# Kernel tuning notes

Measured on AMD Instinct MI355X. Metric: run time of the kernel, lower is better.

Reference implementation:

```python
import jax, jax.numpy as jnp
import numpy as np

B, CH, H, W = 128, 3, 224, 224
R = 14
S = R * R  # 196 superpixels
DIMS = [11, 96, 192, 384, 768, 768]
BN_EPS = 1e-5


def setup_inputs() -> dict:
    key = jax.random.key(0)
    ks = jax.random.split(key, 64)
    inp = {}
    inp["x"] = jax.random.normal(ks[0], (B, CH, H, W), jnp.float32)
    inp["sliced"] = jax.random.randint(ks[1], (B, H, W), 0, S, jnp.int32)
    ki = 2
    for i in range(5):
        ci, co = DIMS[i], DIMS[i + 1]
        inp[f"w{i}"] = jax.random.normal(ks[ki], (co, ci), jnp.float32) / np.sqrt(ci); ki += 1
        inp[f"b{i}"] = jnp.zeros((co,), jnp.float32)
        inp[f"g{i}"] = jnp.ones((co,), jnp.float32)
        inp[f"be{i}"] = jnp.zeros((co,), jnp.float32)
        inp[f"rm{i}"] = jax.random.normal(ks[ki], (co,), jnp.float32) * 0.1; ki += 1
        inp[f"rv{i}"] = jax.random.uniform(ks[ki], (co,), jnp.float32) + 0.5; ki += 1
    return inp


def _seg_features(x, sliced):
    # x: [B,3,H,W] float, sliced: [B,H,W] int labels in [0,S)
    b, c, h, w = x.shape
    n = h * w
    ids = sliced.reshape(b, n).astype(jnp.int32)
    gid = (jnp.arange(b, dtype=jnp.int32)[:, None] * S + ids).reshape(-1)  # [B*N]

    counts = jax.ops.segment_sum(jnp.ones((b * n,), x.dtype), gid, num_segments=b * S)  # [B*S]
    rows = jnp.repeat(jnp.arange(h, dtype=x.dtype), w)
    cols = jnp.tile(jnp.arange(w, dtype=x.dtype), h)
    coords = jnp.stack([rows, cols], -1)                       # [N,2]
    coords_b = jnp.broadcast_to(coords, (b, n, 2)).reshape(b * n, 2)
    coord_sum = jax.ops.segment_sum(coords_b, gid, num_segments=b * S)  # [B*S,2]

    rgb = x.reshape(b, c, n).transpose(0, 2, 1).reshape(b * n, c)       # [B*N,3]
    rgb_sum = jax.ops.segment_sum(rgb, gid, num_segments=b * S)
    rgb_sq = jax.ops.segment_sum(rgb * rgb, gid, num_segments=b * S)

    cnt = counts[:, None]
    safe = jnp.maximum(cnt, 1.0)
    mean_coord = coord_sum / safe                              # [B*S,2]
    mean_rgb = rgb_sum / safe                                  # [B*S,3]
    # torch .std is unbiased; NaN (count<=1) replaced by 0
    var = (rgb_sq - cnt * mean_rgb * mean_rgb) / jnp.maximum(cnt - 1.0, 1.0)
    std = jnp.where(cnt > 1.0, jnp.sqrt(jnp.maximum(var, 0.0)), 0.0)

    mc = mean_coord.reshape(b, S, 2)
    mr = mean_rgb.reshape(b, S, 3)
    sd = std.reshape(b, S, 3)
    # gather pixel at the (truncated) mean location of each segment
    ri = jnp.clip(mc[..., 0].astype(jnp.int32), 0, h - 1)      # [B,S]
    ci = jnp.clip(mc[..., 1].astype(jnp.int32), 0, w - 1)
    gathered = x[jnp.arange(b)[:, None], :, ri, ci]            # [B,S,3]

    feat = jnp.concatenate([mc, mr, sd, gathered], -1)         # [B,S,11]
    feat = feat * (counts.reshape(b, S, 1) > 0).astype(x.dtype)  # absent segments stay 0
    return feat.transpose(0, 2, 1).reshape(b, 11, R, R)


def _conv_bn(h, w, b, g, be, rm, rv, act):
    # 1x1 conv == channel contraction
    h = jnp.einsum('bchw,oc->bohw', h, w) + b[None, :, None, None]
    scale = g / jnp.sqrt(rv + BN_EPS)
    h = (h - rm[None, :, None, None]) * scale[None, :, None, None] + be[None, :, None, None]
    return jax.nn.relu(h) if act else h


def reference(x, sliced,
              w0, b0, g0, be0, rm0, rv0,
              w1, b1, g1, be1, rm1, rv1,
              w2, b2, g2, be2, rm2, rv2,
              w3, b3, g3, be3, rm3, rv3,
              w4, b4, g4, be4, rm4, rv4):
    params = [(w0, b0, g0, be0, rm0, rv0), (w1, b1, g1, be1, rm1, rv1),
              (w2, b2, g2, be2, rm2, rv2), (w3, b3, g3, be3, rm3, rv3),
              (w4, b4, g4, be4, rm4, rv4)]
    h = _seg_features(x, sliced)                # [B,11,14,14]
    for i, (w, b, g, be, rm, rv) in enumerate(params):
        h = _conv_bn(h, w, b, g, be, rm, rv, act=(i < 4))  # last block: BN only
    return (sliced, h)
```

## Files before the change

kernel.cpp:

```cpp
#include <hip/hip_runtime.h>
#include <hip/hip_bf16.h>

#define HW    50176
#define IMGW  224
#define SEG   196
#define NBATCH 128
#define NCOL  (NBATCH * SEG)
#define PB    14
#define CHUNK (HW / PB)
#define VCHUNK (CHUNK / 4)

typedef __attribute__((ext_vector_type(8))) short bf16x8;
typedef __attribute__((ext_vector_type(4))) float f32x4;
typedef unsigned long long u64;

static __device__ __forceinline__ ushort f2bf(float v) {
    __hip_bfloat16 h = __float2bfloat16(v);
    return *reinterpret_cast<ushort*>(&h);
}

__global__ __launch_bounds__(256) void seg_accum(const float* __restrict__ x,
                                                 const int*   __restrict__ sl,
                                                 float*       __restrict__ stats) {
    __shared__ u64 ls[4][SEG];
    int b    = blockIdx.x / PB;
    int part = blockIdx.x % PB;
    int tid  = threadIdx.x;

    for (int i = tid; i < 4 * SEG; i += 256) (&ls[0][0])[i] = 0ull;
    __syncthreads();

    const float* xb = x + (size_t)b * 3 * HW;
    const int*   sb = sl + (size_t)b * HW;
    int v0 = part * VCHUNK;

    for (int vi = tid; vi < VCHUNK; vi += 256) {
        int vg = v0 + vi;
        int4   id4 = ((const int4*)sb)[vg];
        float4 r4  = ((const float4*)xb)[vg];
        float4 g4  = ((const float4*)(xb + HW))[vg];
        float4 b4  = ((const float4*)(xb + 2 * HW))[vg];
        int p   = vg * 4;
        int row = p / IMGW;
        int col = p - row * IMGW;
        u64 rowbits = ((u64)1 << 48) | ((u64)(unsigned)row << 24);

#pragma unroll
        for (int q = 0; q < 4; ++q) {
            int   id = (q == 0) ? id4.x : (q == 1) ? id4.y : (q == 2) ? id4.z : id4.w;
            float r  = (q == 0) ? r4.x  : (q == 1) ? r4.y  : (q == 2) ? r4.z  : r4.w;
            float g  = (q == 0) ? g4.x  : (q == 1) ? g4.y  : (q == 2) ? g4.z  : g4.w;
            float bl = (q == 0) ? b4.x  : (q == 1) ? b4.y  : (q == 2) ? b4.z  : b4.w;

            unsigned qr  = (unsigned)fmaf(r,  8192.f, 131072.5f);
            unsigned qg  = (unsigned)fmaf(g,  8192.f, 131072.5f);
            unsigned qb  = (unsigned)fmaf(bl, 8192.f, 131072.5f);
            unsigned qr2 = (unsigned)fmaf(r * r,  2048.f, 0.5f);
            unsigned qg2 = (unsigned)fmaf(g * g,  2048.f, 0.5f);
            unsigned qb2 = (unsigned)fmaf(bl * bl, 2048.f, 0.5f);

            atomicAdd(&ls[0][id], rowbits | (unsigned)(col + q));
            atomicAdd(&ls[1][id], ((u64)qg  << 32) | qr);
            atomicAdd(&ls[2][id], ((u64)qr2 << 32) | qb);
            atomicAdd(&ls[3][id], ((u64)qb2 << 32) | qg2);
        }
    }
    __syncthreads();

    const float inv_s = 1.f / 8192.f, inv_q = 1.f / 2048.f;
    for (int i = tid; i < SEG; i += 256) {
        u64 v0p = ls[0][i];
        unsigned cnt = (unsigned)(v0p >> 48);
        if (!cnt) continue;
        float fc   = (float)cnt;
        float rows = (float)((unsigned)(v0p >> 24) & 0xFFFFFFu);
        float cols = (float)((unsigned)v0p & 0xFFFFFFu);
        u64 v1 = ls[1][i], v2 = ls[2][i], v3 = ls[3][i];
        float bias = 16.f * fc;
        float rsum = (float)(unsigned)v1         * inv_s - bias;
        float gsum = (float)(unsigned)(v1 >> 32) * inv_s - bias;
        float bsum = (float)(unsigned)v2         * inv_s - bias;
        float rsq  = (float)(unsigned)(v2 >> 32) * inv_q;
        float gsq  = (float)(unsigned)v3         * inv_q;
        float bsq  = (float)(unsigned)(v3 >> 32) * inv_q;

        size_t base = (size_t)b * SEG + i;
        atomicAdd(&stats[0 * NCOL + base], fc);
        atomicAdd(&stats[1 * NCOL + base], rows);
        atomicAdd(&stats[2 * NCOL + base], cols);
        atomicAdd(&stats[3 * NCOL + base], rsum);
        atomicAdd(&stats[4 * NCOL + base], gsum);
        atomicAdd(&stats[5 * NCOL + base], bsum);
        atomicAdd(&stats[6 * NCOL + base], rsq);
        atomicAdd(&stats[7 * NCOL + base], gsq);
        atomicAdd(&stats[8 * NCOL + base], bsq);
    }
}

__global__ __launch_bounds__(256) void feat_build(const float* __restrict__ x,
                                                  const float* __restrict__ stats,
                                                  ushort*      __restrict__ F) {
    int n = blockIdx.x * 256 + threadIdx.x;
    if (n >= NCOL) return;
    int b = n / SEG;

    float cnt  = stats[n];
    float safe = fmaxf(cnt, 1.f);
    float inv  = 1.f / safe;
    float mrow = stats[1 * NCOL + n] * inv;
    float mcol = stats[2 * NCOL + n] * inv;
    float mr   = stats[3 * NCOL + n] * inv;
    float mg   = stats[4 * NCOL + n] * inv;
    float mb   = stats[5 * NCOL + n] * inv;
    float den  = fmaxf(cnt - 1.f, 1.f);
    float vr = (stats[6 * NCOL + n] - cnt * mr * mr) / den;
    float vg = (stats[7 * NCOL + n] - cnt * mg * mg) / den;
    float vb = (stats[8 * NCOL + n] - cnt * mb * mb) / den;
    bool  has2 = cnt > 1.f;
    float sr = has2 ? sqrtf(fmaxf(vr, 0.f)) : 0.f;
    float sg = has2 ? sqrtf(fmaxf(vg, 0.f)) : 0.f;
    float sb = has2 ? sqrtf(fmaxf(vb, 0.f)) : 0.f;

    int ri = min(max((int)mrow, 0), IMGW - 1);
    int ci = min(max((int)mcol, 0), IMGW - 1);
    const float* xb = x + (size_t)b * 3 * HW;
    int pi = ri * IMGW + ci;
    float gr = xb[pi], gg = xb[HW + pi], gb = xb[2 * HW + pi];

    float mask = cnt > 0.f ? 1.f : 0.f;
    ushort* Fr = F + (size_t)n * 64;
#pragma unroll
    for (int k = 11; k < 64; ++k) Fr[k] = 0;
    Fr[0]  = f2bf(mrow * mask);
    Fr[1]  = f2bf(mcol * mask);
    Fr[2]  = f2bf(mr * mask);
    Fr[3]  = f2bf(mg * mask);
    Fr[4]  = f2bf(mb * mask);
    Fr[5]  = f2bf(sr * mask);
    Fr[6]  = f2bf(sg * mask);
    Fr[7]  = f2bf(sb * mask);
    Fr[8]  = f2bf(gr * mask);
    Fr[9]  = f2bf(gg * mask);
    Fr[10] = f2bf(gb * mask);
}

__global__ __launch_bounds__(256) void convert_w(const float* __restrict__ src,
                                                 ushort* __restrict__ dst,
                                                 int Cout, int K, int Kpad, int total) {
    int i = blockIdx.x * 256 + threadIdx.x;
    if (i >= total) return;
    int o = i / Kpad, k = i - o * Kpad;
    float v = (o < Cout && k < K) ? src[(size_t)o * K + k] : 0.f;
    dst[i] = f2bf(v);
}

__global__ __launch_bounds__(256) void gemm_mfma(const ushort* __restrict__ Aact,
                                                 const ushort* __restrict__ Wb,
                                                 void* __restrict__ outp,
                                                 const float* __restrict__ bias,
                                                 const float* __restrict__ gam,
                                                 const float* __restrict__ bet,
                                                 const float* __restrict__ rm,
                                                 const float* __restrict__ rv,
                                                 int Kpad, int Cout, int OutStride,
                                                 int act, int final_out) {
    __shared__ ushort As[128 * 64];
    __shared__ ushort Bs[128 * 64];

    int tid  = threadIdx.x;
    int lane = tid & 63;
    int wid  = tid >> 6;
    int wm   = wid & 1;
    int wn   = wid >> 1;
    int n0   = blockIdx.x * 128;
    int o0   = blockIdx.y * 128;
    int mrow = lane & 15;
    int quad = lane >> 4;
    int swz  = mrow & 7;

    f32x4 acc[4][4];
#pragma unroll
    for (int i = 0; i < 4; ++i)
#pragma unroll
        for (int j = 0; j < 4; ++j) acc[i][j] = (f32x4){0.f, 0.f, 0.f, 0.f};

    int ktiles = Kpad >> 6;
    for (int kt = 0; kt < ktiles; ++kt) {
        int kb = kt * 64;
#pragma unroll
        for (int p = 0; p < 4; ++p) {
            int flat = p * 256 + tid;
            int row = flat >> 3, kg = flat & 7;
            int kgs = kg ^ (row & 7);
            const ushort* gp = Aact + (size_t)(n0 + row) * Kpad + kb + kgs * 8;
            __builtin_amdgcn_global_load_lds(
                (const __attribute__((address_space(1))) void*)gp,
                (__attribute__((address_space(3))) void*)(As + (size_t)(p * 256 + wid * 64) * 8),
                16, 0, 0);
        }
#pragma unroll
        for (int p = 0; p < 4; ++p) {
            int flat = p * 256 + tid;
            int row = flat >> 3, kg = flat & 7;
            int kgs = kg ^ (row & 7);
            const ushort* gp = Wb + (size_t)(o0 + row) * Kpad + kb + kgs * 8;
            __builtin_amdgcn_global_load_lds(
                (const __attribute__((address_space(1))) void*)gp,
                (__attribute__((address_space(3))) void*)(Bs + (size_t)(p * 256 + wid * 64) * 8),
                16, 0, 0);
        }
        __syncthreads();

#pragma unroll
        for (int ks = 0; ks < 2; ++ks) {
            bf16x8 af[4], bfr[4];
            int gbase = ks * 4 + quad;
            int slot  = (gbase ^ swz) * 8;
#pragma unroll
            for (int i = 0; i < 4; ++i)
                af[i] = *(const bf16x8*)&As[(size_t)(wm * 64 + i * 16 + mrow) * 64 + slot];
#pragma unroll
            for (int j = 0; j < 4; ++j)
                bfr[j] = *(const bf16x8*)&Bs[(size_t)(wn * 64 + j * 16 + mrow) * 64 + slot];
#pragma unroll
            for (int i = 0; i < 4; ++i)
#pragma unroll
                for (int j = 0; j < 4; ++j)
                    acc[i][j] = __builtin_amdgcn_mfma_f32_16x16x32_bf16(af[i], bfr[j], acc[i][j], 0, 0, 0);
        }
        __syncthreads();
    }

#pragma unroll
    for (int j = 0; j < 4; ++j) {
        int o = o0 + wn * 64 + j * 16 + mrow;
        float al = 0.f, bt = 0.f;
        if (o < Cout) {
            float sc = gam[o] / sqrtf(rv[o] + 1e-5f);
            al = sc;
            bt = (bias[o] - rm[o]) * sc + bet[o];
        }
#pragma unroll
        for (int i = 0; i < 4; ++i) {
            int nbase = n0 + wm * 64 + i * 16 + quad * 4;
#pragma unroll
            for (int r = 0; r < 4; ++r) {
                float v = acc[i][j][r] * al + bt;
                if (act) v = fmaxf(v, 0.f);
                int n = nbase + r;
                if (final_out) {
                    int b = n / SEG, s = n - b * SEG;
                    ((float*)outp)[(size_t)b * 768 * SEG + (size_t)o * SEG + s] = v;
                } else {
                    ((ushort*)outp)[(size_t)n * OutStride + o] = f2bf(v);
                }
            }
        }
    }
}

__global__ __launch_bounds__(256) void copy_sliced(const int4* __restrict__ sl,
                                                   float4* __restrict__ out) {
    int i = blockIdx.x * 256 + threadIdx.x;
    int4 v = sl[i];
    out[i] = make_float4((float)v.x, (float)v.y, (float)v.z, (float)v.w);
}

extern "C" void kernel_launch(void* const* d_in, const int* in_sizes, int n_in,
                              void* d_out, int out_size, void* d_ws, size_t ws_size,
                              hipStream_t stream) {
    const float* x  = (const float*)d_in[0];
    const int*   sl = (const int*)d_in[1];
    const float* Wp[5], *Bp[5], *Gp[5], *BEp[5], *RMp[5], *RVp[5];
    for (int i = 0; i < 5; ++i) {
        Wp[i]  = (const float*)d_in[2 + 6 * i + 0];
        Bp[i]  = (const float*)d_in[2 + 6 * i + 1];
        Gp[i]  = (const float*)d_in[2 + 6 * i + 2];
        BEp[i] = (const float*)d_in[2 + 6 * i + 3];
        RMp[i] = (const float*)d_in[2 + 6 * i + 4];
        RVp[i] = (const float*)d_in[2 + 6 * i + 5];
    }
    float* out = (float*)d_out;

    const int Kpad[5]  = {64, 128, 256, 384, 768};
    const int Kreal[5] = {11, 96, 192, 384, 768};
    const int Cout[5]  = {96, 192, 384, 768, 768};
    const int Opad[5]  = {128, 256, 384, 768, 768};

    char* wsb = (char*)d_ws;
    float*  stats = (float*)wsb;
    wsb += (size_t)9 * NCOL * sizeof(float);
    ushort* F = (ushort*)wsb;
    wsb += (size_t)NCOL * 64 * sizeof(ushort);
    ushort* Wpad[5];
    for (int i = 0; i < 5; ++i) {
        Wpad[i] = (ushort*)wsb;
        wsb += (size_t)Opad[i] * Kpad[i] * sizeof(ushort);
    }
    ushort* bufA = (ushort*)wsb;
    wsb += (size_t)NCOL * 384 * sizeof(ushort);
    ushort* bufB = (ushort*)wsb;

    hipMemsetAsync(stats, 0, (size_t)9 * NCOL * sizeof(float), stream);

    for (int i = 0; i < 5; ++i) {
        int total = Opad[i] * Kpad[i];
        convert_w<<<(total + 255) / 256, 256, 0, stream>>>(
            Wp[i], Wpad[i], Cout[i], Kreal[i], Kpad[i], total);
    }

    seg_accum<<<NBATCH * PB, 256, 0, stream>>>(x, sl, stats);
    feat_build<<<(NCOL + 255) / 256, 256, 0, stream>>>(x, stats, F);

    const int NT = NCOL / 128;
    gemm_mfma<<<dim3(NT, Opad[0] / 128), 256, 0, stream>>>(
        F, Wpad[0], bufA, Bp[0], Gp[0], BEp[0], RMp[0], RVp[0],
        Kpad[0], Cout[0], Opad[0], 1, 0);
    gemm_mfma<<<dim3(NT, Opad[1] / 128), 256, 0, stream>>>(
        bufA, Wpad[1], bufB, Bp[1], Gp[1], BEp[1], RMp[1], RVp[1],
        Kpad[1], Cout[1], Opad[1], 1, 0);
    gemm_mfma<<<dim3(NT, Opad[2] / 128), 256, 0, stream>>>(
        bufB, Wpad[2], bufA, Bp[2], Gp[2], BEp[2], RMp[2], RVp[2],
        Kpad[2], Cout[2], Opad[2], 1, 0);
    gemm_mfma<<<dim3(NT, Opad[3] / 128), 256, 0, stream>>>(
        bufA, Wpad[3], bufB, Bp[3], Gp[3], BEp[3], RMp[3], RVp[3],
        Kpad[3], Cout[3], Opad[3], 1, 0);
    gemm_mfma<<<dim3(NT, Opad[4] / 128), 256, 0, stream>>>(
        bufB, Wpad[4], out + (size_t)NBATCH * HW, Bp[4], Gp[4], BEp[4], RMp[4], RVp[4],
        Kpad[4], Cout[4], 0, 0, 1);

    copy_sliced<<<(NBATCH * HW / 4) / 256, 256, 0, stream>>>((const int4*)sl,
                                                             (float4*)out);
}
```

Before: 411.7 us.

## Double-buffer GEMM LDS tiles and remap workgroups across XCDs

The MFMA GEMM now keeps two LDS buffers per operand, so the next k-tile's global_load_lds runs while the current tile is being multiplied. This replaces two barriers per iteration with one waitcnt plus barrier. Workgroup ids are also remapped so that consecutive logical tiles land on the same XCD, aiming for better L2 reuse. The cost is double the LDS use (64KB per block), which may lower occupancy. The waitcnt-before-barrier ordering also has to be correct for the loads that bypass registers and go straight to LDS.

After: 413.1 us. Within noise of the previous version (+0.3%).

```diff
diff --git a/kernel.cpp b/kernel.cpp
--- a/kernel.cpp
+++ b/kernel.cpp
@@ -164,16 +164,26 @@
                                                  const float* __restrict__ rv,
                                                  int Kpad, int Cout, int OutStride,
                                                  int act, int final_out) {
-    __shared__ ushort As[128 * 64];
-    __shared__ ushort Bs[128 * 64];
+    __shared__ ushort As[2][128 * 64];
+    __shared__ ushort Bs[2][128 * 64];
 
     int tid  = threadIdx.x;
     int lane = tid & 63;
     int wid  = tid >> 6;
     int wm   = wid & 1;
     int wn   = wid >> 1;
-    int n0   = blockIdx.x * 128;
-    int o0   = blockIdx.y * 128;
+
+    int nbx  = gridDim.x, nby = gridDim.y;
+    int nwg  = nbx * nby;
+    int orig = blockIdx.y * nbx + blockIdx.x;
+    int xcd  = orig & 7;
+    int q    = nwg >> 3, r = nwg & 7;
+    int wgid = (xcd < r ? xcd * (q + 1) : r * (q + 1) + (xcd - r) * q) + (orig >> 3);
+    int bx   = wgid / nby;
+    int by   = wgid - bx * nby;
+    int n0   = bx * 128;
+    int o0   = by * 128;
+
     int mrow = lane & 15;
     int quad = lane >> 4;
     int swz  = mrow & 7;
@@ -184,33 +194,36 @@
 #pragma unroll
         for (int j = 0; j < 4; ++j) acc[i][j] = (f32x4){0.f, 0.f, 0.f, 0.f};
 
-    int ktiles = Kpad >> 6;
-    for (int kt = 0; kt < ktiles; ++kt) {
+    const ushort* aSrc[4];
+    const ushort* bSrc[4];
+    int ldsDst[4];
+#pragma unroll
+    for (int p = 0; p < 4; ++p) {
+        int flat = p * 256 + tid;
+        int row  = flat >> 3, kg = flat & 7;
+        int kgs  = kg ^ (row & 7);
+        aSrc[p]  = Aact + (size_t)(n0 + row) * Kpad + kgs * 8;
+        bSrc[p]  = Wb   + (size_t)(o0 + row) * Kpad + kgs * 8;
+        ldsDst[p] = (p * 256 + wid * 64) * 8;
+    }
+
+    auto stage = [&](int buf, int kt) {
         int kb = kt * 64;
 #pragma unroll
-        for (int p = 0; p < 4; ++p) {
-            int flat = p * 256 + tid;
-            int row = flat >> 3, kg = flat & 7;
-            int kgs = kg ^ (row & 7);
-            const ushort* gp = Aact + (size_t)(n0 + row) * Kpad + kb + kgs * 8;
+        for (int p = 0; p < 4; ++p)
             __builtin_amdgcn_global_load_lds(
-                (const __attribute__((address_space(1))) void*)gp,
-                (__attribute__((address_space(3))) void*)(As + (size_t)(p * 256 + wid * 64) * 8),
+                (const __attribute__((address_space(1))) void*)(aSrc[p] + kb),
+                (__attribute__((address_space(3))) void*)(&As[buf][ldsDst[p]]),
                 16, 0, 0);
-        }
-#pragma unroll
-        for (int p = 0; p < 4; ++p) {
-            int flat = p * 256 + tid;
-            int row = flat >> 3, kg = flat & 7;
-            int kgs = kg ^ (row & 7);
-            const ushort* gp = Wb + (size_t)(o0 + row) * Kpad + kb + kgs * 8;
+#pragma unroll
+        for (int p = 0; p < 4; ++p)
             __builtin_amdgcn_global_load_lds(
-                (const __attribute__((address_space(1))) void*)gp,
-                (__attribute__((address_space(3))) void*)(Bs + (size_t)(p * 256 + wid * 64) * 8),
+                (const __attribute__((address_space(1))) void*)(bSrc[p] + kb),
+                (__attribute__((address_space(3))) void*)(&Bs[buf][ldsDst[p]]),
                 16, 0, 0);
-        }
-        __syncthreads();
-
+    };
+
+    auto compute = [&](int buf) {
 #pragma unroll
         for (int ks = 0; ks < 2; ++ks) {
             bf16x8 af[4], bfr[4];
@@ -218,18 +231,33 @@
             int slot  = (gbase ^ swz) * 8;
 #pragma unroll
             for (int i = 0; i < 4; ++i)
-                af[i] = *(const bf16x8*)&As[(size_t)(wm * 64 + i * 16 + mrow) * 64 + slot];
+                af[i] = *(const bf16x8*)&As[buf][(size_t)(wm * 64 + i * 16 + mrow) * 64 + slot];
 #pragma unroll
             for (int j = 0; j < 4; ++j)
-                bfr[j] = *(const bf16x8*)&Bs[(size_t)(wn * 64 + j * 16 + mrow) * 64 + slot];
+                bfr[j] = *(const bf16x8*)&Bs[buf][(size_t)(wn * 64 + j * 16 + mrow) * 64 + slot];
 #pragma unroll
             for (int i = 0; i < 4; ++i)
 #pragma unroll
                 for (int j = 0; j < 4; ++j)
                     acc[i][j] = __builtin_amdgcn_mfma_f32_16x16x32_bf16(af[i], bfr[j], acc[i][j], 0, 0, 0);
         }
-        __syncthreads();
-    }
+    };
+
+    int ktiles = Kpad >> 6;
+
+    stage(0, 0);
+    asm volatile("s_waitcnt vmcnt(0)" ::: "memory");
+    __builtin_amdgcn_s_barrier();
+
+    int cur = 0;
+    for (int t = 0; t < ktiles - 1; ++t) {
+        stage(cur ^ 1, t + 1);
+        compute(cur);
+        asm volatile("s_waitcnt vmcnt(0)" ::: "memory");
+        __builtin_amdgcn_s_barrier();
+        cur ^= 1;
+    }
+    compute(cur);
 
 #pragma unroll
     for (int j = 0; j < 4; ++j) {
@@ -244,10 +272,10 @@
         for (int i = 0; i < 4; ++i) {
             int nbase = n0 + wm * 64 + i * 16 + quad * 4;
 #pragma unroll
-            for (int r = 0; r < 4; ++r) {
-                float v = acc[i][j][r] * al + bt;
+            for (int rr = 0; rr < 4; ++rr) {
+                float v = acc[i][j][rr] * al + bt;
                 if (act) v = fmaxf(v, 0.f);
-                int n = nbase + r;
+                int n = nbase + rr;
                 if (final_out) {
                     int b = n / SEG, s = n - b * SEG;
                     ((float*)outp)[(size_t)b * 768 * SEG + (size_t)o * SEG + s] = v;
```
